# Performance work log

Hardware: AMD Instinct MI355X
Metric: run time of the kernel (lower is better)

The kernel has to match this reference:

```python
import jax, jax.numpy as jnp
import numpy as np


def setup_inputs() -> dict:
    key = jax.random.key(0)
    k1, k2 = jax.random.split(key)
    N, D, E = 16384, 4096, 64  # tokens, n_embd, n_exp
    x = jax.random.normal(k1, (N, D), dtype=jnp.float32)
    W = jax.random.normal(k2, (E, D), dtype=jnp.float32) * 0.02  # w_gate weight [n_exp, n_embd]
    return {"x": x, "W": W, "top_k": 4, "n_groups": 8, "n_limited_groups": 4}


def reference(x, W, top_k, n_groups, n_limited_groups):
    ROUTE_SCALE = 1.0
    N = x.shape[0]
    E = W.shape[0]
    exp_per_group = E // n_groups

    logits = x @ W.T                      # [N, E] gate linear (bias=False)
    scores = jax.nn.softmax(logits, -1)   # func == 'softmax'

    # group-limited routing: pick top n_limited_groups groups by max score (bias=False path)
    gs = scores.reshape(N, n_groups, exp_per_group)
    group_scores = gs.max(axis=-1)                             # [N, G]
    _, top_grp = jax.lax.top_k(group_scores, n_limited_groups)  # [N, L]
    selected = jnp.any(
        jnp.arange(n_groups)[None, None, :] == top_grp[:, :, None], axis=1
    )                                                           # [N, G] bool
    masked = jnp.where(selected[:, :, None], gs, -jnp.inf).reshape(N, E)

    # top-k experts over unmasked scores; weights are the gathered scores
    topk_vals, topk_idx = jax.lax.top_k(masked, top_k)          # [N, K]
    weights = (topk_vals * ROUTE_SCALE).astype(x.dtype)         # softmax -> no renorm

    # histc over expert ids
    counts = jnp.zeros((E,), jnp.int32).at[topk_idx.reshape(-1)].add(1)
    return weights, topk_idx, counts
```

## Files before the change

kernel.cpp:

```cpp
#include <hip/hip_runtime.h>
#include <math.h>

#define NTOK 16384
#define DDIM 4096
#define NEXP 64
#define KTOP 4

#define SPLITK 4
#define KPER (DDIM / SPLITK)
#define BK 32
#define NSTG (KPER / BK)
#define TPB 128
#define NBLK ((NTOK / TPB) * SPLITK)

typedef __attribute__((ext_vector_type(8))) short short8;
typedef __attribute__((ext_vector_type(4))) float f32x4;


__device__ __forceinline__ unsigned short f2bf_rtn(float x) {
    unsigned int b = __float_as_uint(x);
    return (unsigned short)((b + 0x7FFFu + ((b >> 16) & 1u)) >> 16);
}
__device__ __forceinline__ float bf2f(unsigned short h) {
    return __uint_as_float(((unsigned int)h) << 16);
}
__device__ __forceinline__ short8 mk8(unsigned int a, unsigned int b,
                                      unsigned int c, unsigned int d) {
    union { unsigned int u[4]; short8 s; } p;
    p.u[0] = a; p.u[1] = b; p.u[2] = c; p.u[3] = d;
    return p.s;
}
__device__ __forceinline__ void gl2lds16(const void* g, void* l) {
    __builtin_amdgcn_global_load_lds(
        (const __attribute__((address_space(1))) unsigned int*)g,
        (__attribute__((address_space(3))) unsigned int*)l, 16, 0, 0);
}

__global__ __launch_bounds__(256) void prep_kernel(
    const float* __restrict__ W, unsigned short* __restrict__ Whi,
    unsigned short* __restrict__ Wlo, float* __restrict__ counts)
{
    int idx = blockIdx.x * 256 + threadIdx.x;
    float x = W[idx];
    unsigned short h = f2bf_rtn(x);
    float lo = x - bf2f(h);
    Whi[idx] = h;
    Wlo[idx] = f2bf_rtn(lo);
    if (blockIdx.x == 0 && threadIdx.x < NEXP) counts[threadIdx.x] = 0.0f;
}

__global__ __launch_bounds__(512, 4) void gemm_kernel(
    const float* __restrict__ X, const unsigned short* __restrict__ Whi,
    const unsigned short* __restrict__ Wlo, float* __restrict__ part)
{
    __shared__ float          sX[3][TPB * BK];
    __shared__ unsigned short sH[3][NEXP * BK];
    __shared__ unsigned short sL[3][NEXP * BK];

    const int tid  = threadIdx.x;
    const int lane = tid & 63;
    const int w    = tid >> 6;
    const int tb   = blockIdx.x >> 2;
    const int s    = blockIdx.x & 3;
    const int kbase = s * KPER;
    const int tok0 = tb * TPB;

    const int r0 = (w * 2    ) * 8 + (lane >> 3);
    const int r1 = (w * 2 + 1) * 8 + (lane >> 3);
    const int xp = lane & 7;
    const float* xsrc0 = X + (size_t)(tok0 + r0) * DDIM + kbase + ((xp ^ (r0 & 7)) << 2);
    const float* xsrc1 = X + (size_t)(tok0 + r1) * DDIM + kbase + ((xp ^ (r1 & 7)) << 2);
    const int xdst0 = (w * 2    ) * 256;
    const int xdst1 = (w * 2 + 1) * 256;

    const unsigned short* const wtab_src = (w < 4) ? Whi : Wlo;
    const int eb = w & 3;
    const int we = eb * 16 + (lane & 15);
    const unsigned short* wsrc = wtab_src + (size_t)we * DDIM + kbase + (lane >> 4) * 8;
    const int wdst = eb * 512 + lane * 8;
    unsigned short (* const wtab_dst)[NEXP * BK] = (w < 4) ? sH : sL;

#define ISSUE(st_, slot_)                                                   \
    {                                                                       \
        gl2lds16(xsrc0 + (st_) * BK, &sX[slot_][xdst0]);                    \
        gl2lds16(xsrc1 + (st_) * BK, &sX[slot_][xdst1]);                    \
        gl2lds16(wsrc  + (st_) * BK, &wtab_dst[slot_][wdst]);               \
    }

    ISSUE(0, 0)
    ISSUE(1, 1)
    __syncthreads();

    const int fr = lane & 15;
    const int fg = lane >> 4;
    const int aoff = (w * 16 + fr) * BK;
    const int akey = fr & 7;

    f32x4 acc[4];
    #pragma unroll
    for (int ng = 0; ng < 4; ++ng) acc[ng] = (f32x4){0.f, 0.f, 0.f, 0.f};

    #pragma unroll
    for (int st = 0; st < NSTG; ++st) {
        const int slot = st % 3;

        if (st + 2 < NSTG) ISSUE(st + 2, (st + 2) % 3)

        const float4 qa = *(const float4*)&sX[slot][aoff + (((fg * 2    ) ^ akey) << 2)];
        const float4 qb = *(const float4*)&sX[slot][aoff + (((fg * 2 + 1) ^ akey) << 2)];

        const unsigned int u0 = __float_as_uint(qa.x), u1 = __float_as_uint(qa.y);
        const unsigned int u2 = __float_as_uint(qa.z), u3 = __float_as_uint(qa.w);
        const unsigned int u4 = __float_as_uint(qb.x), u5 = __float_as_uint(qb.y);
        const unsigned int u6 = __float_as_uint(qb.z), u7 = __float_as_uint(qb.w);
        const short8 ahi = mk8((u0 >> 16) | (u1 & 0xFFFF0000u),
                               (u2 >> 16) | (u3 & 0xFFFF0000u),
                               (u4 >> 16) | (u5 & 0xFFFF0000u),
                               (u6 >> 16) | (u7 & 0xFFFF0000u));
        const float l0 = qa.x - __uint_as_float(u0 & 0xFFFF0000u);
        const float l1 = qa.y - __uint_as_float(u1 & 0xFFFF0000u);
        const float l2 = qa.z - __uint_as_float(u2 & 0xFFFF0000u);
        const float l3 = qa.w - __uint_as_float(u3 & 0xFFFF0000u);
        const float l4 = qb.x - __uint_as_float(u4 & 0xFFFF0000u);
        const float l5 = qb.y - __uint_as_float(u5 & 0xFFFF0000u);
        const float l6 = qb.z - __uint_as_float(u6 & 0xFFFF0000u);
        const float l7 = qb.w - __uint_as_float(u7 & 0xFFFF0000u);
        const short8 alo = mk8(
            (__float_as_uint(l0) >> 16) | (__float_as_uint(l1) & 0xFFFF0000u),
            (__float_as_uint(l2) >> 16) | (__float_as_uint(l3) & 0xFFFF0000u),
            (__float_as_uint(l4) >> 16) | (__float_as_uint(l5) & 0xFFFF0000u),
            (__float_as_uint(l6) >> 16) | (__float_as_uint(l7) & 0xFFFF0000u));

        #pragma unroll
        for (int ng = 0; ng < 4; ++ng) {
            const int bo = ng * 512 + fg * 128 + fr * 8;
            const short8 bh = *(const short8*)&sH[slot][bo];
            const short8 bl = *(const short8*)&sL[slot][bo];
            acc[ng] = __builtin_amdgcn_mfma_f32_16x16x32_bf16(ahi, bh, acc[ng], 0, 0, 0);
            acc[ng] = __builtin_amdgcn_mfma_f32_16x16x32_bf16(ahi, bl, acc[ng], 0, 0, 0);
            acc[ng] = __builtin_amdgcn_mfma_f32_16x16x32_bf16(alo, bh, acc[ng], 0, 0, 0);
        }

        if (st < NSTG - 1) {
            if (st < NSTG - 2) {
                asm volatile("s_waitcnt vmcnt(3)" ::: "memory");
            } else {
                asm volatile("s_waitcnt vmcnt(0)" ::: "memory");
            }
            __builtin_amdgcn_sched_barrier(0);
            __builtin_amdgcn_s_barrier();
        }
    }
#undef ISSUE

    #pragma unroll
    for (int r = 0; r < 4; ++r) {
        const int n = tok0 + w * 16 + fg * 4 + r;
        float* __restrict__ pp = part + ((size_t)n * SPLITK + s) * NEXP;
        #pragma unroll
        for (int ng = 0; ng < 4; ++ng)
            pp[ng * 16 + fr] = acc[ng][r];
    }
}

__global__ __launch_bounds__(256) void route_kernel(
    const float* __restrict__ part, float* __restrict__ outW,
    float* __restrict__ outI, float* __restrict__ counts)
{
    __shared__ int hist[NEXP];
    const int tid = threadIdx.x;
    if (tid < NEXP) hist[tid] = 0;
    __syncthreads();

    const int lane = tid & 63;
    const int wv   = tid >> 6;
    const int tok_base = blockIdx.x * 32 + wv * 8;

    for (int t = 0; t < 8; ++t) {
        const int n = tok_base + t;
        float L = 0.0f;
        #pragma unroll
        for (int s = 0; s < SPLITK; ++s)
            L += part[((size_t)n * SPLITK + s) * NEXP + lane];

        float m = L;
        #pragma unroll
        for (int off = 32; off > 0; off >>= 1) m = fmaxf(m, __shfl_xor(m, off));
        float p = expf(L - m);
        float ssum = p;
        #pragma unroll
        for (int off = 32; off > 0; off >>= 1) ssum += __shfl_xor(ssum, off);
        const float score = p / ssum;

        float gm = score;
        gm = fmaxf(gm, __shfl_xor(gm, 1));
        gm = fmaxf(gm, __shfl_xor(gm, 2));
        gm = fmaxf(gm, __shfl_xor(gm, 4));

        float ga[8];
        #pragma unroll
        for (int g = 0; g < 8; ++g) ga[g] = __shfl(gm, g * 8);
        unsigned selmask = 0u;
        #pragma unroll
        for (int r = 0; r < 4; ++r) {
            float best = -INFINITY; int bg = 0;
            #pragma unroll
            for (int g = 0; g < 8; ++g) {
                bool taken  = (selmask >> g) & 1u;
                bool better = (!taken) && (ga[g] > best);
                bg   = better ? g : bg;
                best = better ? ga[g] : best;
            }
            selmask |= (1u << bg);
        }

        float ms = ((selmask >> (lane >> 3)) & 1u) ? score : -INFINITY;
        float wk[4]; int wi[4];
        #pragma unroll
        for (int r = 0; r < 4; ++r) {
            float v = ms; int ix = lane;
            #pragma unroll
            for (int off = 32; off > 0; off >>= 1) {
                float vo = __shfl_xor(v, off);
                int   io = __shfl_xor(ix, off);
                if (vo > v || (vo == v && io < ix)) { v = vo; ix = io; }
            }
            wk[r] = v; wi[r] = ix;
            if (lane == ix) ms = -INFINITY;
        }

        if (lane == 0) {
            *(float4*)&outW[(size_t)n * 4] = make_float4(wk[0], wk[1], wk[2], wk[3]);
            *(float4*)&outI[(size_t)n * 4] =
                make_float4((float)wi[0], (float)wi[1], (float)wi[2], (float)wi[3]);
            atomicAdd(&hist[wi[0]], 1);
            atomicAdd(&hist[wi[1]], 1);
            atomicAdd(&hist[wi[2]], 1);
            atomicAdd(&hist[wi[3]], 1);
        }
    }

    __syncthreads();
    if (tid < NEXP) atomicAdd(&counts[tid], (float)hist[tid]);
}

extern "C" void kernel_launch(void* const* d_in, const int* in_sizes, int n_in,
                              void* d_out, int out_size, void* d_ws, size_t ws_size,
                              hipStream_t stream) {
    const float* X = (const float*)d_in[0];
    const float* W = (const float*)d_in[1];

    float* outW   = (float*)d_out;
    float* outI   = outW + (size_t)NTOK * KTOP;
    float* counts = outW + (size_t)2 * NTOK * KTOP;

    float*          part = (float*)d_ws;
    unsigned short* Whi  = (unsigned short*)(part + (size_t)NTOK * SPLITK * NEXP);
    unsigned short* Wlo  = Whi + (size_t)NEXP * DDIM;

    prep_kernel<<<(NEXP * DDIM) / 256, 256, 0, stream>>>(W, Whi, Wlo, counts);
    gemm_kernel<<<NBLK, 512, 0, stream>>>(X, Whi, Wlo, part);
    route_kernel<<<NTOK / 32, 256, 0, stream>>>(part, outW, outI, counts);
}
```

Measured before the change: 108.2 us.

## Restructure gate GEMM to split-K 16 with register-resident prepacked weights

The gate GEMM moves from a 4-way split-K, 3-stage LDS pipeline to a 16-way split-K. Each block loads its whole 64-token by 256-wide X slice into LDS in one shot. The bf16 hi/lo weights are prepacked by the prep kernel into MFMA fragment order and loaded straight into registers, so weight traffic no longer goes through LDS. Byte extraction now uses a perm intrinsic. The aim is more parallelism and less per-stage barrier overhead, at the cost of four times the partial-sum traffic through the workspace, a larger workspace, and no load/compute overlap inside a block.

```diff
diff --git a/kernel.cpp b/kernel.cpp
--- a/kernel.cpp
+++ b/kernel.cpp
@@ -6,12 +6,11 @@
 #define NEXP 64
 #define KTOP 4
 
-#define SPLITK 4
-#define KPER (DDIM / SPLITK)
-#define BK 32
-#define NSTG (KPER / BK)
-#define TPB 128
+#define SPLITK 16
+#define KPER 256
+#define TPB 64
 #define NBLK ((NTOK / TPB) * SPLITK)
+#define WP_HL 262144
 
 typedef __attribute__((ext_vector_type(8))) short short8;
 typedef __attribute__((ext_vector_type(4))) float f32x4;
@@ -23,144 +22,124 @@
 }
 __device__ __forceinline__ float bf2f(unsigned short h) {
     return __uint_as_float(((unsigned int)h) << 16);
-}
-__device__ __forceinline__ short8 mk8(unsigned int a, unsigned int b,
-                                      unsigned int c, unsigned int d) {
-    union { unsigned int u[4]; short8 s; } p;
-    p.u[0] = a; p.u[1] = b; p.u[2] = c; p.u[3] = d;
-    return p.s;
 }
 __device__ __forceinline__ void gl2lds16(const void* g, void* l) {
     __builtin_amdgcn_global_load_lds(
         (const __attribute__((address_space(1))) unsigned int*)g,
         (__attribute__((address_space(3))) unsigned int*)l, 16, 0, 0);
 }
+__device__ __forceinline__ unsigned int pack_hi(unsigned int u0, unsigned int u1) {
+    return __builtin_amdgcn_perm(u1, u0, 0x07060302u);
+}
 
 __global__ __launch_bounds__(256) void prep_kernel(
-    const float* __restrict__ W, unsigned short* __restrict__ Whi,
-    unsigned short* __restrict__ Wlo, float* __restrict__ counts)
+    const float* __restrict__ W, unsigned short* __restrict__ Wp,
+    float* __restrict__ counts)
 {
     int idx = blockIdx.x * 256 + threadIdx.x;
+    int e = idx >> 12, d = idx & 4095;
     float x = W[idx];
     unsigned short h = f2bf_rtn(x);
     float lo = x - bf2f(h);
-    Whi[idx] = h;
-    Wlo[idx] = f2bf_rtn(lo);
+    int s = d >> 8, p = (d >> 3) & 31, i = d & 7;
+    size_t o = (((size_t)s * 32 + p) * 64 + e) * 8 + i;
+    Wp[o]         = h;
+    Wp[WP_HL + o] = f2bf_rtn(lo);
     if (blockIdx.x == 0 && threadIdx.x < NEXP) counts[threadIdx.x] = 0.0f;
 }
 
 __global__ __launch_bounds__(512, 4) void gemm_kernel(
-    const float* __restrict__ X, const unsigned short* __restrict__ Whi,
-    const unsigned short* __restrict__ Wlo, float* __restrict__ part)
+    const float* __restrict__ X, const unsigned short* __restrict__ Wp,
+    float* __restrict__ part)
 {
-    __shared__ float          sX[3][TPB * BK];
-    __shared__ unsigned short sH[3][NEXP * BK];
-    __shared__ unsigned short sL[3][NEXP * BK];
+    __shared__ float sX[TPB * KPER];
 
     const int tid  = threadIdx.x;
     const int lane = tid & 63;
     const int w    = tid >> 6;
-    const int tb   = blockIdx.x >> 2;
-    const int s    = blockIdx.x & 3;
+    const int qm   = w >> 2;
+    const int qn   = w & 3;
+    const int tb   = blockIdx.x >> 4;
+    const int s    = blockIdx.x & 15;
     const int kbase = s * KPER;
     const int tok0 = tb * TPB;
 
-    const int r0 = (w * 2    ) * 8 + (lane >> 3);
-    const int r1 = (w * 2 + 1) * 8 + (lane >> 3);
-    const int xp = lane & 7;
-    const float* xsrc0 = X + (size_t)(tok0 + r0) * DDIM + kbase + ((xp ^ (r0 & 7)) << 2);
-    const float* xsrc1 = X + (size_t)(tok0 + r1) * DDIM + kbase + ((xp ^ (r1 & 7)) << 2);
-    const int xdst0 = (w * 2    ) * 256;
-    const int xdst1 = (w * 2 + 1) * 256;
-
-    const unsigned short* const wtab_src = (w < 4) ? Whi : Wlo;
-    const int eb = w & 3;
-    const int we = eb * 16 + (lane & 15);
-    const unsigned short* wsrc = wtab_src + (size_t)we * DDIM + kbase + (lane >> 4) * 8;
-    const int wdst = eb * 512 + lane * 8;
-    unsigned short (* const wtab_dst)[NEXP * BK] = (w < 4) ? sH : sL;
-
-#define ISSUE(st_, slot_)                                                   \
-    {                                                                       \
-        gl2lds16(xsrc0 + (st_) * BK, &sX[slot_][xdst0]);                    \
-        gl2lds16(xsrc1 + (st_) * BK, &sX[slot_][xdst1]);                    \
-        gl2lds16(wsrc  + (st_) * BK, &wtab_dst[slot_][wdst]);               \
-    }
-
-    ISSUE(0, 0)
-    ISSUE(1, 1)
-    __syncthreads();
+    #pragma unroll
+    for (int i = 0; i < 8; ++i) {
+        const int r = w * 8 + i;
+        const float* src = X + (size_t)(tok0 + r) * DDIM + kbase
+                         + ((lane ^ (r & 7)) << 2);
+        gl2lds16(src, &sX[r * KPER]);
+    }
 
     const int fr = lane & 15;
     const int fg = lane >> 4;
-    const int aoff = (w * 16 + fr) * BK;
-    const int akey = fr & 7;
-
-    f32x4 acc[4];
-    #pragma unroll
-    for (int ng = 0; ng < 4; ++ng) acc[ng] = (f32x4){0.f, 0.f, 0.f, 0.f};
-
-    #pragma unroll
-    for (int st = 0; st < NSTG; ++st) {
-        const int slot = st % 3;
-
-        if (st + 2 < NSTG) ISSUE(st + 2, (st + 2) % 3)
-
-        const float4 qa = *(const float4*)&sX[slot][aoff + (((fg * 2    ) ^ akey) << 2)];
-        const float4 qb = *(const float4*)&sX[slot][aoff + (((fg * 2 + 1) ^ akey) << 2)];
-
-        const unsigned int u0 = __float_as_uint(qa.x), u1 = __float_as_uint(qa.y);
-        const unsigned int u2 = __float_as_uint(qa.z), u3 = __float_as_uint(qa.w);
-        const unsigned int u4 = __float_as_uint(qb.x), u5 = __float_as_uint(qb.y);
-        const unsigned int u6 = __float_as_uint(qb.z), u7 = __float_as_uint(qb.w);
-        const short8 ahi = mk8((u0 >> 16) | (u1 & 0xFFFF0000u),
-                               (u2 >> 16) | (u3 & 0xFFFF0000u),
-                               (u4 >> 16) | (u5 & 0xFFFF0000u),
-                               (u6 >> 16) | (u7 & 0xFFFF0000u));
-        const float l0 = qa.x - __uint_as_float(u0 & 0xFFFF0000u);
-        const float l1 = qa.y - __uint_as_float(u1 & 0xFFFF0000u);
-        const float l2 = qa.z - __uint_as_float(u2 & 0xFFFF0000u);
-        const float l3 = qa.w - __uint_as_float(u3 & 0xFFFF0000u);
-        const float l4 = qb.x - __uint_as_float(u4 & 0xFFFF0000u);
-        const float l5 = qb.y - __uint_as_float(u5 & 0xFFFF0000u);
-        const float l6 = qb.z - __uint_as_float(u6 & 0xFFFF0000u);
-        const float l7 = qb.w - __uint_as_float(u7 & 0xFFFF0000u);
-        const short8 alo = mk8(
-            (__float_as_uint(l0) >> 16) | (__float_as_uint(l1) & 0xFFFF0000u),
-            (__float_as_uint(l2) >> 16) | (__float_as_uint(l3) & 0xFFFF0000u),
-            (__float_as_uint(l4) >> 16) | (__float_as_uint(l5) & 0xFFFF0000u),
-            (__float_as_uint(l6) >> 16) | (__float_as_uint(l7) & 0xFFFF0000u));
-
-        #pragma unroll
-        for (int ng = 0; ng < 4; ++ng) {
-            const int bo = ng * 512 + fg * 128 + fr * 8;
-            const short8 bh = *(const short8*)&sH[slot][bo];
-            const short8 bl = *(const short8*)&sL[slot][bo];
-            acc[ng] = __builtin_amdgcn_mfma_f32_16x16x32_bf16(ahi, bh, acc[ng], 0, 0, 0);
-            acc[ng] = __builtin_amdgcn_mfma_f32_16x16x32_bf16(ahi, bl, acc[ng], 0, 0, 0);
-            acc[ng] = __builtin_amdgcn_mfma_f32_16x16x32_bf16(alo, bh, acc[ng], 0, 0, 0);
-        }
-
-        if (st < NSTG - 1) {
-            if (st < NSTG - 2) {
-                asm volatile("s_waitcnt vmcnt(3)" ::: "memory");
-            } else {
-                asm volatile("s_waitcnt vmcnt(0)" ::: "memory");
-            }
-            __builtin_amdgcn_sched_barrier(0);
-            __builtin_amdgcn_s_barrier();
-        }
-    }
-#undef ISSUE
-
-    #pragma unroll
-    for (int r = 0; r < 4; ++r) {
-        const int n = tok0 + w * 16 + fg * 4 + r;
-        float* __restrict__ pp = part + ((size_t)n * SPLITK + s) * NEXP;
-        #pragma unroll
-        for (int ng = 0; ng < 4; ++ng)
-            pp[ng * 16 + fr] = acc[ng][r];
-    }
+    const size_t e8 = (size_t)(qn * 16 + fr) * 8;
+    short8 bh[8], bl[8];
+    #pragma unroll
+    for (int ks = 0; ks < 8; ++ks) {
+        const size_t o = ((size_t)(s * 32 + ks * 4 + fg)) * 512 + e8;
+        bh[ks] = *(const short8*)(Wp + o);
+        bl[ks] = *(const short8*)(Wp + WP_HL + o);
+    }
+
+    __syncthreads();
+
+    const int key = fr & 7;
+    int baseA[2][2];
+    #pragma unroll
+    for (int mg = 0; mg < 2; ++mg) {
+        const int row = qm * 32 + mg * 16 + fr;
+        baseA[mg][0] = row * KPER + (((fg * 2    ) ^ key) << 2);
+        baseA[mg][1] = row * KPER + (((fg * 2 + 1) ^ key) << 2);
+    }
+
+    f32x4 acc[2];
+    acc[0] = (f32x4){0.f, 0.f, 0.f, 0.f};
+    acc[1] = (f32x4){0.f, 0.f, 0.f, 0.f};
+
+    #pragma unroll
+    for (int ks = 0; ks < 8; ++ks) {
+        #pragma unroll
+        for (int mg = 0; mg < 2; ++mg) {
+            const float4 qa = *(const float4*)&sX[baseA[mg][0] + ks * 32];
+            const float4 qb = *(const float4*)&sX[baseA[mg][1] + ks * 32];
+
+            const unsigned int u0 = __float_as_uint(qa.x), u1 = __float_as_uint(qa.y);
+            const unsigned int u2 = __float_as_uint(qa.z), u3 = __float_as_uint(qa.w);
+            const unsigned int u4 = __float_as_uint(qb.x), u5 = __float_as_uint(qb.y);
+            const unsigned int u6 = __float_as_uint(qb.z), u7 = __float_as_uint(qb.w);
+            union { unsigned int u[4]; short8 s8; } ah, al;
+            ah.u[0] = pack_hi(u0, u1);
+            ah.u[1] = pack_hi(u2, u3);
+            ah.u[2] = pack_hi(u4, u5);
+            ah.u[3] = pack_hi(u6, u7);
+            const float l0 = qa.x - __uint_as_float(u0 & 0xFFFF0000u);
+            const float l1 = qa.y - __uint_as_float(u1 & 0xFFFF0000u);
+            const float l2 = qa.z - __uint_as_float(u2 & 0xFFFF0000u);
+            const float l3 = qa.w - __uint_as_float(u3 & 0xFFFF0000u);
+            const float l4 = qb.x - __uint_as_float(u4 & 0xFFFF0000u);
+            const float l5 = qb.y - __uint_as_float(u5 & 0xFFFF0000u);
+            const float l6 = qb.z - __uint_as_float(u6 & 0xFFFF0000u);
+            const float l7 = qb.w - __uint_as_float(u7 & 0xFFFF0000u);
+            al.u[0] = pack_hi(__float_as_uint(l0), __float_as_uint(l1));
+            al.u[1] = pack_hi(__float_as_uint(l2), __float_as_uint(l3));
+            al.u[2] = pack_hi(__float_as_uint(l4), __float_as_uint(l5));
+            al.u[3] = pack_hi(__float_as_uint(l6), __float_as_uint(l7));
+
+            acc[mg] = __builtin_amdgcn_mfma_f32_16x16x32_bf16(ah.s8, bh[ks], acc[mg], 0, 0, 0);
+            acc[mg] = __builtin_amdgcn_mfma_f32_16x16x32_bf16(ah.s8, bl[ks], acc[mg], 0, 0, 0);
+            acc[mg] = __builtin_amdgcn_mfma_f32_16x16x32_bf16(al.s8, bh[ks], acc[mg], 0, 0, 0);
+        }
+    }
+
+    #pragma unroll
+    for (int mg = 0; mg < 2; ++mg)
+        #pragma unroll
+        for (int r = 0; r < 4; ++r) {
+            const int n = tok0 + qm * 32 + mg * 16 + fg * 4 + r;
+            part[((size_t)n * SPLITK + s) * NEXP + qn * 16 + fr] = acc[mg][r];
+        }
 }
 
 __global__ __launch_bounds__(256) void route_kernel(
@@ -255,10 +234,9 @@
     float* counts = outW + (size_t)2 * NTOK * KTOP;
 
     float*          part = (float*)d_ws;
-    unsigned short* Whi  = (unsigned short*)(part + (size_t)NTOK * SPLITK * NEXP);
-    unsigned short* Wlo  = Whi + (size_t)NEXP * DDIM;
-
-    prep_kernel<<<(NEXP * DDIM) / 256, 256, 0, stream>>>(W, Whi, Wlo, counts);
-    gemm_kernel<<<NBLK, 512, 0, stream>>>(X, Whi, Wlo, part);
+    unsigned short* Wp   = (unsigned short*)(part + (size_t)NTOK * SPLITK * NEXP);
+
+    prep_kernel<<<(NEXP * DDIM) / 256, 256, 0, stream>>>(W, Wp, counts);
+    gemm_kernel<<<NBLK, 512, 0, stream>>>(X, Wp, part);
     route_kernel<<<NTOK / 32, 256, 0, stream>>>(part, outW, outI, counts);
 }
```

Measured after the change: 119.8 us. 1.11x slower.
